# Optimization experiments

Hardware: AMD Instinct MI355X
Metric: run time of the kernel (lower is better)

Reference implementation:

```python
import jax, jax.numpy as jnp
import numpy as np

B, S, E, H = 4, 2048, 512, 8
DH = E // H
EPS = 1e-5

def _ln(x, g, b):
    m = jnp.mean(x, axis=-1, keepdims=True)
    v = jnp.var(x, axis=-1, keepdims=True)
    return (x - m) * jax.lax.rsqrt(v + EPS) * g + b

def setup_inputs() -> dict:
    key = jax.random.key(0)
    ks = jax.random.split(key, 8)
    sc = 0.02
    return {
        "x": jax.random.normal(ks[0], (B, S, E), dtype=jnp.float32),
        "ln1_g": jnp.ones((E,), jnp.float32),
        "ln1_b": jnp.zeros((E,), jnp.float32),
        "in_proj_w": sc * jax.random.normal(ks[1], (3 * E, E), jnp.float32),
        "in_proj_b": jnp.zeros((3 * E,), jnp.float32),
        "out_w": sc * jax.random.normal(ks[2], (E, E), jnp.float32),
        "out_b": jnp.zeros((E,), jnp.float32),
        "ln2_g": jnp.ones((E,), jnp.float32),
        "ln2_b": jnp.zeros((E,), jnp.float32),
        "fc1_w": sc * jax.random.normal(ks[3], (E, E), jnp.float32),
        "fc1_b": jnp.zeros((E,), jnp.float32),
        "fc2_w": sc * jax.random.normal(ks[4], (E, E), jnp.float32),
        "fc2_b": jnp.zeros((E,), jnp.float32),
    }

def reference(x, ln1_g, ln1_b, in_proj_w, in_proj_b, out_w, out_b,
              ln2_g, ln2_b, fc1_w, fc1_b, fc2_w, fc2_b):
    # pre-LN
    z = _ln(x, ln1_g, ln1_b)
    # qkv projection (torch MHA packed in_proj: [3E, E])
    qkv = z @ in_proj_w.T + in_proj_b          # [B,S,3E]
    q, k, v = jnp.split(qkv, 3, axis=-1)
    q = q.reshape(B, S, H, DH)
    k = k.reshape(B, S, H, DH)
    v = v.reshape(B, S, H, DH)
    scores = jnp.einsum("bqhd,bkhd->bhqk", q, k) / np.sqrt(DH).astype(np.float32)
    causal = jnp.triu(jnp.ones((S, S), dtype=bool), k=1)  # True = masked
    neg = jnp.finfo(scores.dtype).min
    scores = jnp.where(causal, neg, scores)
    attn = jax.nn.softmax(scores, axis=-1)      # [B,H,S,S]
    ctx = jnp.einsum("bhqk,bkhd->bqhd", attn, v).reshape(B, S, E)
    attn_out = ctx @ out_w.T + out_b
    # torch MHA with need_weights=True averages over heads by default
    attn_weights = jnp.mean(attn, axis=1)       # [B,S,S]
    z2 = x + attn_out
    y = _ln(z2, ln2_g, ln2_b)
    y = jax.nn.leaky_relu(y @ fc1_w.T + fc1_b, negative_slope=0.01)
    y = y @ fc2_w.T + fc2_b
    y = y + z2
    return (y, attn_weights)
```

## Files before the change

### kernel.cpp

```cpp
#include <hip/hip_runtime.h>

typedef short bf16x8 __attribute__((ext_vector_type(8)));
typedef float f32x4 __attribute__((ext_vector_type(4)));
typedef unsigned short u16x8 __attribute__((ext_vector_type(8)));

#define NB 4
#define SQ 2048
#define EM 512
#define NH 8
#define DHD 64
#define QSCALE 0.1803368801111731f

__device__ __forceinline__ unsigned short f2bf(float x) {
  unsigned u = __float_as_uint(x);
  u += 0x7FFFu + ((u >> 16) & 1u);
  return (unsigned short)(u >> 16);
}

__device__ __forceinline__ int sw8(int row, int col8) { return col8 ^ ((row & 7) << 3); }
__device__ __forceinline__ int sw32(int row, int lg) { return (lg ^ ((row >> 1) & 3)) * 8; }

__device__ __forceinline__ void glds16(const void* g, void* l) {
  __builtin_amdgcn_global_load_lds(
      (const __attribute__((address_space(1))) void*)g,
      (__attribute__((address_space(3))) void*)l, 16, 0, 0);
}

__global__ __launch_bounds__(256) void f2bf4_kernel(
    const float* __restrict__ w0, const float* __restrict__ w1,
    const float* __restrict__ w2, const float* __restrict__ w3,
    unsigned short* __restrict__ o0, unsigned short* __restrict__ o1,
    unsigned short* __restrict__ o2, unsigned short* __restrict__ o3) {
  int i = (blockIdx.x * 256 + threadIdx.x) * 8;
  const float* src;
  unsigned short* dst;
  int off;
  if (i < 786432) { src = w0; dst = o0; off = i; }
  else if (i < 1048576) { src = w1; dst = o1; off = i - 786432; }
  else if (i < 1310720) { src = w2; dst = o2; off = i - 1048576; }
  else { src = w3; dst = o3; off = i - 1310720; }
  f32x4 a = *(const f32x4*)(src + off);
  f32x4 b = *(const f32x4*)(src + off + 4);
  u16x8 o;
#pragma unroll
  for (int j = 0; j < 4; ++j) { o[j] = f2bf(a[j]); o[j + 4] = f2bf(b[j]); }
  *(u16x8*)(dst + off) = o;
}

__global__ __launch_bounds__(256) void ln_kernel(const float* __restrict__ x,
                                                 const float* __restrict__ g,
                                                 const float* __restrict__ bb,
                                                 unsigned short* __restrict__ out) {
  int tid = threadIdx.x;
  int row = blockIdx.x * 4 + (tid >> 6);
  int lane = tid & 63;
  size_t base = (size_t)row * EM + lane * 8;
  f32x4 v0 = *(const f32x4*)(x + base);
  f32x4 v1 = *(const f32x4*)(x + base + 4);
  float s = 0.f, q = 0.f;
#pragma unroll
  for (int j = 0; j < 4; ++j) { s += v0[j] + v1[j]; q += v0[j] * v0[j] + v1[j] * v1[j]; }
#pragma unroll
  for (int m = 1; m < 64; m <<= 1) { s += __shfl_xor(s, m); q += __shfl_xor(q, m); }
  float mean = s * (1.f / EM);
  float var = q * (1.f / EM) - mean * mean;
  float rs = rsqrtf(var + 1e-5f);
  f32x4 g0 = *(const f32x4*)(g + lane * 8), g1 = *(const f32x4*)(g + lane * 8 + 4);
  f32x4 b0 = *(const f32x4*)(bb + lane * 8), b1 = *(const f32x4*)(bb + lane * 8 + 4);
  u16x8 o;
#pragma unroll
  for (int j = 0; j < 4; ++j) {
    o[j] = f2bf((v0[j] - mean) * rs * g0[j] + b0[j]);
    o[j + 4] = f2bf((v1[j] - mean) * rs * g1[j] + b1[j]);
  }
  *(u16x8*)(out + base) = o;
}

template <bool LEAKY, bool RESID, bool OUTF32>
__global__ __launch_bounds__(256) void gemm64b(
    const unsigned short* __restrict__ A, const unsigned short* __restrict__ Bm,
    const float* __restrict__ bias, const float* __restrict__ resid,
    float* __restrict__ outf, unsigned short* __restrict__ outh, int N, int K) {
  __shared__ unsigned short As[2][64][32];
  __shared__ unsigned short Bs[2][64][32];
  int lin = blockIdx.x;
  int xcd = lin & 7, idx = lin >> 3;
  int m0 = (xcd * 16 + (idx & 15)) * 64;
  int n0 = (idx >> 4) * 64;
  int t = threadIdx.x;
  int wv = t >> 6, ln = t & 63, lg = ln >> 4, lr = ln & 15;
  int row16 = ln >> 2;
  int chs = ((ln & 3) ^ ((row16 >> 1) & 3)) * 8;
  f32x4 acc[4];
#pragma unroll
  for (int c = 0; c < 4; ++c)
#pragma unroll
    for (int r = 0; r < 4; ++r) acc[c][r] = 0.f;

  const unsigned short* ag = A + (size_t)(m0 + wv * 16 + row16) * K + chs;
  const unsigned short* bg = Bm + (size_t)(n0 + wv * 16 + row16) * K + chs;

  glds16(ag, &As[0][wv * 16][0]);
  glds16(bg, &Bs[0][wv * 16][0]);

  int nk = K >> 5;
  for (int ki = 0; ki < nk; ++ki) {
    int cur = ki & 1;
    __syncthreads();
    if (ki + 1 < nk) {
      int nb = cur ^ 1;
      int ko_ = (ki + 1) * 32;
      glds16(ag + ko_, &As[nb][wv * 16][0]);
      glds16(bg + ko_, &Bs[nb][wv * 16][0]);
    }
    int arw = wv * 16 + lr;
    bf16x8 af = *(const bf16x8*)&As[cur][arw][sw32(arw, lg)];
#pragma unroll
    for (int c = 0; c < 4; ++c) {
      int brw = c * 16 + lr;
      bf16x8 bf = *(const bf16x8*)&Bs[cur][brw][sw32(brw, lg)];
      acc[c] = __builtin_amdgcn_mfma_f32_16x16x32_bf16(af, bf, acc[c], 0, 0, 0);
    }
  }
#pragma unroll
  for (int c = 0; c < 4; ++c) {
    int C_ = n0 + c * 16 + lr;
    float bv = bias[C_];
#pragma unroll
    for (int r = 0; r < 4; ++r) {
      int R_ = m0 + wv * 16 + lg * 4 + r;
      float v = acc[c][r] + bv;
      if (LEAKY) v = v > 0.f ? v : 0.01f * v;
      if (RESID) v += resid[(size_t)R_ * N + C_];
      if (OUTF32) {
        outf[(size_t)R_ * N + C_] = v;
      } else {
        outh[(size_t)R_ * N + C_] = f2bf(v);
      }
    }
  }
}

__global__ __launch_bounds__(256) void gemm128qkv(
    const unsigned short* __restrict__ A, const unsigned short* __restrict__ Bm,
    const float* __restrict__ bias, unsigned short* __restrict__ qo,
    unsigned short* __restrict__ ko, unsigned short* __restrict__ vo, int K) {
  __shared__ unsigned short As[2][128][32];
  __shared__ unsigned short Bs[2][128][32];
  int lin = blockIdx.x;
  int xcd = lin & 7, idx = lin >> 3;
  int m0 = (xcd * 8 + (idx & 7)) * 128;
  int n0 = (idx >> 3) * 128;
  int t = threadIdx.x;
  int wv = t >> 6, ln = t & 63, lg = ln >> 4, lr = ln & 15;
  int wr = wv >> 1, wc = wv & 1;
  int row16 = ln >> 2, chunk = (ln & 3) * 8;
  f32x4 acc[4][4];
#pragma unroll
  for (int m = 0; m < 4; ++m)
#pragma unroll
    for (int n = 0; n < 4; ++n)
#pragma unroll
      for (int r = 0; r < 4; ++r) acc[m][n][r] = 0.f;

  const unsigned short* agA = A + (size_t)(m0 + wv * 16 + row16) * K + chunk;
  const unsigned short* agB = A + (size_t)(m0 + 64 + wv * 16 + row16) * K + chunk;
  const unsigned short* bgA = Bm + (size_t)(n0 + wv * 16 + row16) * K + chunk;
  const unsigned short* bgB = Bm + (size_t)(n0 + 64 + wv * 16 + row16) * K + chunk;

  glds16(agA, &As[0][wv * 16][0]);
  glds16(agB, &As[0][64 + wv * 16][0]);
  glds16(bgA, &Bs[0][wv * 16][0]);
  glds16(bgB, &Bs[0][64 + wv * 16][0]);

  int nk = K >> 5;
  for (int ki = 0; ki < nk; ++ki) {
    int cur = ki & 1;
    __syncthreads();
    if (ki + 1 < nk) {
      int nb = cur ^ 1;
      int ko_ = (ki + 1) * 32;
      glds16(agA + ko_, &As[nb][wv * 16][0]);
      glds16(agB + ko_, &As[nb][64 + wv * 16][0]);
      glds16(bgA + ko_, &Bs[nb][wv * 16][0]);
      glds16(bgB + ko_, &Bs[nb][64 + wv * 16][0]);
    }
    bf16x8 af[4], bfr[4];
#pragma unroll
    for (int m = 0; m < 4; ++m)
      af[m] = *(const bf16x8*)&As[cur][wr * 64 + m * 16 + lr][lg * 8];
#pragma unroll
    for (int n = 0; n < 4; ++n)
      bfr[n] = *(const bf16x8*)&Bs[cur][wc * 64 + n * 16 + lr][lg * 8];
#pragma unroll
    for (int m = 0; m < 4; ++m)
#pragma unroll
      for (int n = 0; n < 4; ++n)
        acc[m][n] = __builtin_amdgcn_mfma_f32_16x16x32_bf16(af[m], bfr[n], acc[m][n], 0, 0, 0);
  }

#pragma unroll
  for (int n = 0; n < 4; ++n) {
    int C_ = n0 + wc * 64 + n * 16 + lr;
    float bv = bias[C_];
#pragma unroll
    for (int m = 0; m < 4; ++m) {
#pragma unroll
      for (int r = 0; r < 4; ++r) {
        int R_ = m0 + wr * 64 + m * 16 + lg * 4 + r;
        float v = acc[m][n][r] + bv;
        int which = C_ >> 9, f = C_ & 511, h = f >> 6, d = f & 63;
        int b_ = R_ >> 11, s_ = R_ & 2047;
        if (which == 0) {
          qo[(((size_t)b_ * NH + h) * SQ + s_) * DHD + d] = f2bf(v * QSCALE);
        } else if (which == 1) {
          ko[(((size_t)b_ * NH + h) * SQ + s_) * DHD + d] = f2bf(v);
        } else {
          vo[(((size_t)b_ * NH + h) * DHD + d) * SQ + s_] = f2bf(v);
        }
      }
    }
  }
}

__global__ __launch_bounds__(256) void flash_kernel(
    const unsigned short* __restrict__ Q, const unsigned short* __restrict__ Kb,
    const unsigned short* __restrict__ Vt, unsigned short* __restrict__ ctx,
    float* __restrict__ mstat, float* __restrict__ lstat) {
  __shared__ unsigned short Ks[2][64][64];
  __shared__ unsigned short Vs[2][64][64];
  __shared__ unsigned short Ps[4][16][64];
  int lin = blockIdx.x;
  int xcd = lin & 7, idx = lin >> 3;
  int qt = 31 - (idx >> 2);
  int grp = xcd + 8 * (idx & 3);
  int h = grp & 7, b = grp >> 3;
  int qb = qt * 64;
  int t = threadIdx.x, wv = t >> 6, ln = t & 63, lg = ln >> 4, lr = ln & 15;
  int rsub = ln >> 3;
  int csw = ((ln & 7) ^ rsub) * 8;
  size_t headoff = ((size_t)b * NH + h) * SQ;
  const unsigned short* kg0 = Kb + (headoff + wv * 16 + rsub) * DHD + csw;
  const unsigned short* kg1 = Kb + (headoff + wv * 16 + 8 + rsub) * DHD + csw;
  const unsigned short* vg0 = Vt + (((size_t)b * NH + h) * DHD + wv * 16 + rsub) * SQ + csw;
  const unsigned short* vg1 = Vt + (((size_t)b * NH + h) * DHD + wv * 16 + 8 + rsub) * SQ + csw;

  const unsigned short* qrow = Q + (headoff + qb + wv * 16 + lr) * DHD;
  bf16x8 aq0 = *(const bf16x8*)(qrow + lg * 8);
  bf16x8 aq1 = *(const bf16x8*)(qrow + 32 + lg * 8);

  bf16x8 vones;
#pragma unroll
  for (int j = 0; j < 8; ++j) vones[j] = (lr == 0) ? (short)0x3F80 : (short)0;

  f32x4 cacc[4], lacc;
#pragma unroll
  for (int nd = 0; nd < 4; ++nd)
#pragma unroll
    for (int r = 0; r < 4; ++r) cacc[nd][r] = 0.f;
#pragma unroll
  for (int r = 0; r < 4; ++r) lacc[r] = 0.f;
  float mrun[4];
#pragma unroll
  for (int r = 0; r < 4; ++r) mrun[r] = -__builtin_inff();

  int nkt = qt + 1;
  glds16(kg0, &Ks[0][wv * 16][0]);
  glds16(kg1, &Ks[0][wv * 16 + 8][0]);
  glds16(vg0, &Vs[0][wv * 16][0]);
  glds16(vg1, &Vs[0][wv * 16 + 8][0]);

  for (int kt = 0; kt < nkt; ++kt) {
    int cur = kt & 1;
    __syncthreads();
    if (kt + 1 < nkt) {
      int nb = cur ^ 1;
      size_t ko_ = (size_t)(kt + 1) * 64;
      glds16(kg0 + ko_ * DHD, &Ks[nb][wv * 16][0]);
      glds16(kg1 + ko_ * DHD, &Ks[nb][wv * 16 + 8][0]);
      glds16(vg0 + ko_, &Vs[nb][wv * 16][0]);
      glds16(vg1 + ko_, &Vs[nb][wv * 16 + 8][0]);
    }

    float sv[4][4];
    __builtin_amdgcn_s_setprio(1);
#pragma unroll
    for (int nt = 0; nt < 4; ++nt) {
      f32x4 sf;
#pragma unroll
      for (int r = 0; r < 4; ++r) sf[r] = 0.f;
      int brw = nt * 16 + lr;
      bf16x8 bk0 = *(const bf16x8*)&Ks[cur][brw][sw8(brw, lg * 8)];
      bf16x8 bk1 = *(const bf16x8*)&Ks[cur][brw][sw8(brw, 32 + lg * 8)];
      sf = __builtin_amdgcn_mfma_f32_16x16x32_bf16(aq0, bk0, sf, 0, 0, 0);
      sf = __builtin_amdgcn_mfma_f32_16x16x32_bf16(aq1, bk1, sf, 0, 0, 0);
#pragma unroll
      for (int r = 0; r < 4; ++r) sv[nt][r] = sf[r];
    }
    __builtin_amdgcn_s_setprio(0);
    if (kt == nkt - 1) {
      int kbase = kt * 64;
#pragma unroll
      for (int nt = 0; nt < 4; ++nt) {
        int kcol = kbase + nt * 16 + lr;
#pragma unroll
        for (int r = 0; r < 4; ++r) {
          int qr = qb + wv * 16 + lg * 4 + r;
          if (kcol > qr) sv[nt][r] = -__builtin_inff();
        }
      }
    }

    float lmax[4];
    bool need = false;
#pragma unroll
    for (int r = 0; r < 4; ++r) {
      lmax[r] = fmaxf(fmaxf(sv[0][r], sv[1][r]), fmaxf(sv[2][r], sv[3][r]));
      need |= (lmax[r] > mrun[r] + 8.f);
    }
    if (__any(need)) {
#pragma unroll
      for (int r = 0; r < 4; ++r) {
        float tm = lmax[r];
#pragma unroll
        for (int m = 1; m < 16; m <<= 1) tm = fmaxf(tm, __shfl_xor(tm, m));
        float mn = fmaxf(mrun[r], tm);
        float sc = exp2f(mrun[r] - mn);
        mrun[r] = mn;
        lacc[r] *= sc;
#pragma unroll
        for (int nd = 0; nd < 4; ++nd) cacc[nd][r] *= sc;
      }
    }
#pragma unroll
    for (int r = 0; r < 4; ++r) {
      int prow = lg * 4 + r;
#pragma unroll
      for (int nt = 0; nt < 4; ++nt) {
        float p = exp2f(sv[nt][r] - mrun[r]);
        Ps[wv][prow][sw8(prow, nt * 16 + lr)] =
            (unsigned short)(__float_as_uint(p) >> 16);
      }
    }

    bf16x8 pf0 = *(const bf16x8*)&Ps[wv][lr][sw8(lr, lg * 8)];
    bf16x8 pf1 = *(const bf16x8*)&Ps[wv][lr][sw8(lr, 32 + lg * 8)];
    __builtin_amdgcn_s_setprio(1);
    lacc = __builtin_amdgcn_mfma_f32_16x16x32_bf16(pf0, vones, lacc, 0, 0, 0);
    lacc = __builtin_amdgcn_mfma_f32_16x16x32_bf16(pf1, vones, lacc, 0, 0, 0);
#pragma unroll
    for (int nd = 0; nd < 4; ++nd) {
      int vrw = nd * 16 + lr;
      bf16x8 vf0 = *(const bf16x8*)&Vs[cur][vrw][sw8(vrw, lg * 8)];
      bf16x8 vf1 = *(const bf16x8*)&Vs[cur][vrw][sw8(vrw, 32 + lg * 8)];
      cacc[nd] = __builtin_amdgcn_mfma_f32_16x16x32_bf16(pf0, vf0, cacc[nd], 0, 0, 0);
      cacc[nd] = __builtin_amdgcn_mfma_f32_16x16x32_bf16(pf1, vf1, cacc[nd], 0, 0, 0);
    }
    __builtin_amdgcn_s_setprio(0);
  }

  float inv[4];
#pragma unroll
  for (int r = 0; r < 4; ++r) inv[r] = 1.f / __shfl(lacc[r], ln & 48);
#pragma unroll
  for (int nd = 0; nd < 4; ++nd)
#pragma unroll
    for (int r = 0; r < 4; ++r) {
      size_t dst = ((size_t)b * SQ + qb + wv * 16 + lg * 4 + r) * EM + h * DHD + nd * 16 + lr;
      ctx[dst] = f2bf(cacc[nd][r] * inv[r]);
    }
  if (lr == 0) {
#pragma unroll
    for (int r = 0; r < 4; ++r) {
      int row = qb + wv * 16 + lg * 4 + r;
      mstat[headoff + row] = mrun[r];
      lstat[headoff + row] = 0.125f * inv[r];
    }
  }
}

__global__ __launch_bounds__(256) void attnw_kernel(
    const unsigned short* __restrict__ Q, const unsigned short* __restrict__ Kb,
    const float* __restrict__ mstat, const float* __restrict__ lstat,
    float* __restrict__ aw) {
  int lin = blockIdx.x;
  int xcd = lin & 7, slot = lin >> 3;
  int combo = xcd + 8 * (slot >> 5);
  int qt = slot & 31;
  int kt2 = combo & 15, b = combo >> 4;
  int qb = qt * 64, kb = kt2 * 128;
  int t = threadIdx.x;
  float* tile = aw + ((size_t)b * SQ + qb) * SQ + kb;
  if (2 * kt2 > qt) {
    int row = t >> 2, cbase = (t & 3) * 32;
    f32x4 z;
#pragma unroll
    for (int j = 0; j < 4; ++j) z[j] = 0.f;
    float* p = tile + (size_t)row * SQ + cbase;
#pragma unroll
    for (int j = 0; j < 8; ++j) *(f32x4*)(p + j * 4) = z;
    return;
  }
  __shared__ unsigned short Ks[2][2][64][64];
  int wv = t >> 6, ln = t & 63, lg = ln >> 4, lr = ln & 15;
  int rsub = ln >> 3;
  int csw = ((ln & 7) ^ rsub) * 8;
  size_t khstride = (size_t)SQ * DHD;
  const unsigned short* kg00 = Kb + (((size_t)b * NH) * SQ + kb + wv * 16 + rsub) * DHD + csw;
  const unsigned short* kg01 = kg00 + (size_t)8 * DHD;
  const unsigned short* kg10 = kg00 + (size_t)64 * DHD;
  const unsigned short* kg11 = kg00 + (size_t)72 * DHD;
  const unsigned short* qg = Q + (((size_t)b * NH) * SQ + qb + wv * 16 + lr) * DHD + lg * 8;
  size_t mbase = (size_t)b * NH * SQ + qb + wv * 16 + lg * 4;

  glds16(kg00, &Ks[0][0][wv * 16][0]);
  glds16(kg01, &Ks[0][0][wv * 16 + 8][0]);
  glds16(kg10, &Ks[0][1][wv * 16][0]);
  glds16(kg11, &Ks[0][1][wv * 16 + 8][0]);

  bf16x8 aqc0 = *(const bf16x8*)qg;
  bf16x8 aqc1 = *(const bf16x8*)(qg + 32);
  bf16x8 aqn0 = *(const bf16x8*)(qg + khstride);
  bf16x8 aqn1 = *(const bf16x8*)(qg + khstride + 32);
  float mmc[4], lic[4], mmn[4], lin_[4];
#pragma unroll
  for (int r = 0; r < 4; ++r) {
    mmc[r] = mstat[mbase + r];
    lic[r] = lstat[mbase + r];
    mmn[r] = mstat[mbase + SQ + r];
    lin_[r] = lstat[mbase + SQ + r];
  }

  f32x4 facc[2][4];
#pragma unroll
  for (int j = 0; j < 2; ++j)
#pragma unroll
    for (int nt = 0; nt < 4; ++nt)
#pragma unroll
      for (int r = 0; r < 4; ++r) facc[j][nt][r] = 0.f;

  for (int h = 0; h < NH; ++h) {
    int cur = h & 1;
    __syncthreads();
    if (h + 1 < NH) {
      size_t ho = (size_t)(h + 1) * khstride;
      glds16(kg00 + ho, &Ks[cur ^ 1][0][wv * 16][0]);
      glds16(kg01 + ho, &Ks[cur ^ 1][0][wv * 16 + 8][0]);
      glds16(kg10 + ho, &Ks[cur ^ 1][1][wv * 16][0]);
      glds16(kg11 + ho, &Ks[cur ^ 1][1][wv * 16 + 8][0]);
    }

#pragma unroll
    for (int nt = 0; nt < 4; ++nt) {
      int brw = nt * 16 + lr;
      f32x4 sf0, sf1;
#pragma unroll
      for (int r = 0; r < 4; ++r) { sf0[r] = 0.f; sf1[r] = 0.f; }
      bf16x8 bk00 = *(const bf16x8*)&Ks[cur][0][brw][sw8(brw, lg * 8)];
      bf16x8 bk01 = *(const bf16x8*)&Ks[cur][0][brw][sw8(brw, 32 + lg * 8)];
      bf16x8 bk10 = *(const bf16x8*)&Ks[cur][1][brw][sw8(brw, lg * 8)];
      bf16x8 bk11 = *(const bf16x8*)&Ks[cur][1][brw][sw8(brw, 32 + lg * 8)];
      sf0 = __builtin_amdgcn_mfma_f32_16x16x32_bf16(aqc0, bk00, sf0, 0, 0, 0);
      sf1 = __builtin_amdgcn_mfma_f32_16x16x32_bf16(aqc0, bk10, sf1, 0, 0, 0);
      sf0 = __builtin_amdgcn_mfma_f32_16x16x32_bf16(aqc1, bk01, sf0, 0, 0, 0);
      sf1 = __builtin_amdgcn_mfma_f32_16x16x32_bf16(aqc1, bk11, sf1, 0, 0, 0);
#pragma unroll
      for (int r = 0; r < 4; ++r) {
        facc[0][nt][r] += exp2f(sf0[r] - mmc[r]) * lic[r];
        facc[1][nt][r] += exp2f(sf1[r] - mmc[r]) * lic[r];
      }
    }

    aqc0 = aqn0; aqc1 = aqn1;
#pragma unroll
    for (int r = 0; r < 4; ++r) { mmc[r] = mmn[r]; lic[r] = lin_[r]; }
    if (h + 2 < NH) {
      aqn0 = *(const bf16x8*)(qg + (size_t)(h + 2) * khstride);
      aqn1 = *(const bf16x8*)(qg + (size_t)(h + 2) * khstride + 32);
#pragma unroll
      for (int r = 0; r < 4; ++r) {
        mmn[r] = mstat[mbase + (size_t)(h + 2) * SQ + r];
        lin_[r] = lstat[mbase + (size_t)(h + 2) * SQ + r];
      }
    }
  }

#pragma unroll
  for (int j = 0; j < 2; ++j) {
    int ktj = 2 * kt2 + j;
    bool fullmask = (ktj > qt);
    bool dg = (ktj == qt);
#pragma unroll
    for (int nt = 0; nt < 4; ++nt) {
      int kc = kb + j * 64 + nt * 16 + lr;
#pragma unroll
      for (int r = 0; r < 4; ++r) {
        int qr = qb + wv * 16 + lg * 4 + r;
        float v = (fullmask || (dg && kc > qr)) ? 0.f : facc[j][nt][r];
        tile[(size_t)(wv * 16 + lg * 4 + r) * SQ + j * 64 + nt * 16 + lr] = v;
      }
    }
  }
}

extern "C" void kernel_launch(void* const* d_in, const int* in_sizes, int n_in,
                              void* d_out, int out_size, void* d_ws, size_t ws_size,
                              hipStream_t stream) {
  (void)in_sizes; (void)n_in; (void)out_size; (void)ws_size;
  const float* x = (const float*)d_in[0];
  const float* ln1g = (const float*)d_in[1];
  const float* ln1b = (const float*)d_in[2];
  const float* wqkv = (const float*)d_in[3];
  const float* bqkv = (const float*)d_in[4];
  const float* wout = (const float*)d_in[5];
  const float* bout = (const float*)d_in[6];
  const float* ln2g = (const float*)d_in[7];
  const float* ln2b = (const float*)d_in[8];
  const float* wfc1 = (const float*)d_in[9];
  const float* bfc1 = (const float*)d_in[10];
  const float* wfc2 = (const float*)d_in[11];
  const float* bfc2 = (const float*)d_in[12];

  char* ws = (char*)d_ws;
  unsigned short* zctx = (unsigned short*)(ws);
  unsigned short* qb_ = (unsigned short*)(ws + 8388608);
  unsigned short* kb_ = (unsigned short*)(ws + 16777216);
  unsigned short* vb_ = (unsigned short*)(ws + 25165824);
  float* z2 = (float*)(ws + 33554432);
  float* mstat = (float*)(ws + 50331648);
  float* lstat = (float*)(ws + 50593792);
  unsigned short* wqkv_h = (unsigned short*)(ws + 50855936);
  unsigned short* wout_h = (unsigned short*)(ws + 52428800);
  unsigned short* wfc1_h = (unsigned short*)(ws + 52953088);
  unsigned short* wfc2_h = (unsigned short*)(ws + 53477376);
  unsigned short* y1 = qb_;
  unsigned short* h1 = kb_;

  float* outy = (float*)d_out;
  float* outw = outy + (size_t)NB * SQ * EM;

  f2bf4_kernel<<<768, 256, 0, stream>>>(wqkv, wout, wfc1, wfc2,
                                        wqkv_h, wout_h, wfc1_h, wfc2_h);

  ln_kernel<<<2048, 256, 0, stream>>>(x, ln1g, ln1b, zctx);
  gemm128qkv<<<768, 256, 0, stream>>>(zctx, wqkv_h, bqkv, qb_, kb_, vb_, 512);
  flash_kernel<<<1024, 256, 0, stream>>>(qb_, kb_, vb_, zctx, mstat, lstat);
  attnw_kernel<<<2048, 256, 0, stream>>>(qb_, kb_, mstat, lstat, outw);
  gemm64b<false, true, true><<<1024, 256, 0, stream>>>(
      zctx, wout_h, bout, x, z2, nullptr, 512, 512);
  ln_kernel<<<2048, 256, 0, stream>>>(z2, ln2g, ln2b, y1);
  gemm64b<true, false, false><<<1024, 256, 0, stream>>>(
      y1, wfc1_h, bfc1, nullptr, nullptr, h1, 512, 512);
  gemm64b<false, true, true><<<1024, 256, 0, stream>>>(
      h1, wfc2_h, bfc2, z2, outy, nullptr, 512, 512);
}
```

Before: 173.4 us.

## Pair query tiles qt and qt+16 per 512-thread block in attention-weights kernel

The attention-weights kernel now runs 512-thread blocks, each covering two query tiles (qpair and qpair+16) against the same 128-key slab. The two halves of the block cooperatively stage the K tiles into shared memory once, which halves K traffic per query tile. Pairing a low tile with a high one also balances causal-mask work across blocks. In exchange, a block whose lower tile is fully masked still runs the QK/exp work for it and then writes zeros, and the larger blocks may lower occupancy flexibility.

```diff
diff --git a/kernel.cpp b/kernel.cpp
--- a/kernel.cpp
+++ b/kernel.cpp
@@ -379,44 +379,44 @@
   }
 }
 
-__global__ __launch_bounds__(256) void attnw_kernel(
+__global__ __launch_bounds__(512) void attnw_kernel(
     const unsigned short* __restrict__ Q, const unsigned short* __restrict__ Kb,
     const float* __restrict__ mstat, const float* __restrict__ lstat,
     float* __restrict__ aw) {
   int lin = blockIdx.x;
   int xcd = lin & 7, slot = lin >> 3;
-  int combo = xcd + 8 * (slot >> 5);
-  int qt = slot & 31;
+  int combo = xcd + 8 * (slot >> 4);
+  int qpair = slot & 15;
   int kt2 = combo & 15, b = combo >> 4;
-  int qb = qt * 64, kb = kt2 * 128;
+  int kb = kt2 * 128;
   int t = threadIdx.x;
-  float* tile = aw + ((size_t)b * SQ + qb) * SQ + kb;
-  if (2 * kt2 > qt) {
-    int row = t >> 2, cbase = (t & 3) * 32;
+  if (2 * kt2 > qpair + 16) {
+    int row = (t & 255) >> 2, cbase = (t & 3) * 32;
+    int qbz = (qpair + (t >> 8) * 16) * 64;
     f32x4 z;
 #pragma unroll
     for (int j = 0; j < 4; ++j) z[j] = 0.f;
-    float* p = tile + (size_t)row * SQ + cbase;
+    float* p = aw + ((size_t)b * SQ + qbz + row) * SQ + kb + cbase;
 #pragma unroll
     for (int j = 0; j < 8; ++j) *(f32x4*)(p + j * 4) = z;
     return;
   }
   __shared__ unsigned short Ks[2][2][64][64];
   int wv = t >> 6, ln = t & 63, lg = ln >> 4, lr = ln & 15;
+  int g = wv >> 2, wq = wv & 3;
+  int qt = qpair + g * 16;
+  int qb = qt * 64;
   int rsub = ln >> 3;
   int csw = ((ln & 7) ^ rsub) * 8;
   size_t khstride = (size_t)SQ * DHD;
-  const unsigned short* kg00 = Kb + (((size_t)b * NH) * SQ + kb + wv * 16 + rsub) * DHD + csw;
-  const unsigned short* kg01 = kg00 + (size_t)8 * DHD;
-  const unsigned short* kg10 = kg00 + (size_t)64 * DHD;
-  const unsigned short* kg11 = kg00 + (size_t)72 * DHD;
-  const unsigned short* qg = Q + (((size_t)b * NH) * SQ + qb + wv * 16 + lr) * DHD + lg * 8;
-  size_t mbase = (size_t)b * NH * SQ + qb + wv * 16 + lg * 4;
-
-  glds16(kg00, &Ks[0][0][wv * 16][0]);
-  glds16(kg01, &Ks[0][0][wv * 16 + 8][0]);
-  glds16(kg10, &Ks[0][1][wv * 16][0]);
-  glds16(kg11, &Ks[0][1][wv * 16 + 8][0]);
+  const unsigned short* kgA =
+      Kb + (((size_t)b * NH) * SQ + kb + g * 64 + wq * 16 + rsub) * DHD + csw;
+  const unsigned short* kgB = kgA + (size_t)8 * DHD;
+  const unsigned short* qg = Q + (((size_t)b * NH) * SQ + qb + wq * 16 + lr) * DHD + lg * 8;
+  size_t mbase = (size_t)b * NH * SQ + qb + wq * 16 + lg * 4;
+
+  glds16(kgA, &Ks[0][g][wq * 16][0]);
+  glds16(kgB, &Ks[0][g][wq * 16 + 8][0]);
 
   bf16x8 aqc0 = *(const bf16x8*)qg;
   bf16x8 aqc1 = *(const bf16x8*)(qg + 32);
@@ -444,10 +444,8 @@
     __syncthreads();
     if (h + 1 < NH) {
       size_t ho = (size_t)(h + 1) * khstride;
-      glds16(kg00 + ho, &Ks[cur ^ 1][0][wv * 16][0]);
-      glds16(kg01 + ho, &Ks[cur ^ 1][0][wv * 16 + 8][0]);
-      glds16(kg10 + ho, &Ks[cur ^ 1][1][wv * 16][0]);
-      glds16(kg11 + ho, &Ks[cur ^ 1][1][wv * 16 + 8][0]);
+      glds16(kgA + ho, &Ks[cur ^ 1][g][wq * 16][0]);
+      glds16(kgB + ho, &Ks[cur ^ 1][g][wq * 16 + 8][0]);
     }
 
 #pragma unroll
@@ -485,6 +483,7 @@
     }
   }
 
+  float* tile = aw + ((size_t)b * SQ + qb) * SQ + kb;
 #pragma unroll
   for (int j = 0; j < 2; ++j) {
     int ktj = 2 * kt2 + j;
@@ -495,9 +494,9 @@
       int kc = kb + j * 64 + nt * 16 + lr;
 #pragma unroll
       for (int r = 0; r < 4; ++r) {
-        int qr = qb + wv * 16 + lg * 4 + r;
+        int qr = qb + wq * 16 + lg * 4 + r;
         float v = (fullmask || (dg && kc > qr)) ? 0.f : facc[j][nt][r];
-        tile[(size_t)(wv * 16 + lg * 4 + r) * SQ + j * 64 + nt * 16 + lr] = v;
+        tile[(size_t)(wq * 16 + lg * 4 + r) * SQ + j * 64 + nt * 16 + lr] = v;
       }
     }
   }
@@ -545,7 +544,7 @@
   ln_kernel<<<2048, 256, 0, stream>>>(x, ln1g, ln1b, zctx);
   gemm128qkv<<<768, 256, 0, stream>>>(zctx, wqkv_h, bqkv, qb_, kb_, vb_, 512);
   flash_kernel<<<1024, 256, 0, stream>>>(qb_, kb_, vb_, zctx, mstat, lstat);
-  attnw_kernel<<<2048, 256, 0, stream>>>(qb_, kb_, mstat, lstat, outw);
+  attnw_kernel<<<1024, 512, 0, stream>>>(qb_, kb_, mstat, lstat, outw);
   gemm64b<false, true, true><<<1024, 256, 0, stream>>>(
       zctx, wout_h, bout, x, z2, nullptr, 512, 512);
   ln_kernel<<<2048, 256, 0, stream>>>(z2, ln2g, ln2b, y1);
```

New measurement: 180.1 us. +3.9%, slower.
